# Optimization experiments

Measured on AMD Instinct MI355X. Metric: run time of the kernel, lower is better.

Reference implementation:

```python
import jax, jax.numpy as jnp
import numpy as np

B, H, W = 32, 768, 768
POS_THR = 0.1
NEG_RATIO = 3
TOPK_NO_POS = 500


def setup_inputs() -> dict:
    key = jax.random.key(0)
    k1, k2, k3 = jax.random.split(key, 3)
    pred = jax.random.uniform(k1, (B, H, W, 2), dtype=jnp.float32)
    region_scores = jax.random.uniform(k2, (B, H, W), dtype=jnp.float32) ** 16
    affinity_scores = jax.random.uniform(k3, (B, H, W), dtype=jnp.float32) ** 16
    return {"pred": pred, "region_scores": region_scores, "affinity_scores": affinity_scores}


def _single_image_loss(pre_loss, label):
    # Vectorized OHEM: replaces the per-sample Python loop + torch.topk.
    b = pre_loss.shape[0]
    loss = pre_loss.reshape(b, -1)   # [B, N]
    lab = label.reshape(b, -1)       # [B, N]
    n = loss.shape[1]
    pos = lab >= POS_THR             # [B, N] bool
    p = jnp.sum(pos, axis=1)         # positive pixel count per sample
    pos_sum = jnp.sum(jnp.where(pos, loss, 0.0), axis=1)
    posi_loss = jnp.where(p > 0, pos_sum / jnp.maximum(p, 1).astype(loss.dtype), 0.0)
    # Negatives sorted descending; -inf pushes positives to the tail.
    # When p == 0 the mask is all-False so this sorts the full loss vector,
    # matching torch.topk(pre_loss[i], 500).
    neg_vals = jnp.where(pos, -jnp.inf, loss)
    sorted_desc = jnp.flip(jnp.sort(neg_vals, axis=1), axis=1)
    nn = n - p                       # negative count
    # mean of all negatives when nn < 3p == mean of top-min(nn,3p); else top-3p
    k = jnp.where(p > 0, jnp.minimum(nn, NEG_RATIO * p), TOPK_NO_POS)
    csum = jnp.cumsum(jnp.where(jnp.isfinite(sorted_desc), sorted_desc, 0.0), axis=1)
    topk_sum = jnp.take_along_axis(csum, jnp.maximum(k - 1, 0)[:, None], axis=1)[:, 0]
    nega_loss = jnp.where(k > 0, topk_sum / jnp.maximum(k, 1).astype(loss.dtype), 0.0)
    return jnp.sum(posi_loss + nega_loss)


def reference(pred, region_scores, affinity_scores):
    p_gh = pred[..., 0]
    p_gah = pred[..., 1]
    loss1 = (p_gh - region_scores) ** 2   # MSELoss(reduction='none')
    loss2 = (p_gah - affinity_scores) ** 2
    char_loss = _single_image_loss(loss1, region_scores)
    affi_loss = _single_image_loss(loss2, affinity_scores)
    b = pred.shape[0]
    return char_loss / b + affi_loss / b
```

## Files before the change

### kernel.cpp

```cpp
#include <hip/hip_runtime.h>


constexpr int   BATCH   = 32;
constexpr int   NPS     = 768 * 768;
constexpr int   CH2     = BATCH * 2;
constexpr int   EPB     = 8192;
constexpr int   BX      = NPS / EPB;
constexpr float POS_THR_F = 0.1f;
constexpr unsigned TOPK_NO_POS = 500u;
constexpr int   NB1     = 2048;
constexpr int   CAP     = 131072;
constexpr int   CAPB    = 1024;

__global__ __launch_bounds__(256, 8) void k_hist(
    const float4* __restrict__ pred4,
    const float4* __restrict__ reg4,
    const float4* __restrict__ aff4,
    unsigned* __restrict__ h1c,
    unsigned* __restrict__ pcnt, float* __restrict__ psum)
{
    __shared__ unsigned sc0[NB1], sc1[NB1];
    __shared__ unsigned wpc[8];
    __shared__ float    wps[8];
    for (int j = threadIdx.x; j < NB1; j += 256) { sc0[j] = 0u; sc1[j] = 0u; }
    __syncthreads();

    const int  b   = blockIdx.y;
    const int  tid = threadIdx.x;
    constexpr int ITERS = EPB / 1024;
    long idx4 = (((long)b * NPS + (long)blockIdx.x * EPB) >> 2) + tid;

    unsigned pc0 = 0, pc1 = 0;
    float    ps0 = 0.f, ps1 = 0.f;

    for (int i = 0; i < ITERS; ++i) {
        const float4 r  = reg4[idx4];
        const float4 a  = aff4[idx4];
        const float4 pA = pred4[idx4 * 2];
        const float4 pB = pred4[idx4 * 2 + 1];
#define DO_PIX(RR, AA, PG, PA) do {                                           \
        float d0 = (PG) - (RR); float v0 = d0 * d0;                           \
        if ((RR) >= POS_THR_F) { pc0++; ps0 += v0; }                          \
        else atomicAdd(&sc0[__float_as_uint(v0) >> 19], 1u);                  \
        float d1 = (PA) - (AA); float v1 = d1 * d1;                           \
        if ((AA) >= POS_THR_F) { pc1++; ps1 += v1; }                          \
        else atomicAdd(&sc1[__float_as_uint(v1) >> 19], 1u);                  \
    } while (0)
        DO_PIX(r.x, a.x, pA.x, pA.y);
        DO_PIX(r.y, a.y, pA.z, pA.w);
        DO_PIX(r.z, a.z, pB.x, pB.y);
        DO_PIX(r.w, a.w, pB.z, pB.w);
#undef DO_PIX
        idx4 += 256;
    }
    __syncthreads();

    for (int j = tid; j < NB1; j += 256) {
        unsigned c0 = sc0[j];
        if (c0) atomicAdd(&h1c[(b*2+0)*NB1 + j], c0);
        unsigned c1 = sc1[j];
        if (c1) atomicAdd(&h1c[(b*2+1)*NB1 + j], c1);
    }
    for (int o = 32; o > 0; o >>= 1) {
        pc0 += __shfl_down(pc0, o); ps0 += __shfl_down(ps0, o);
        pc1 += __shfl_down(pc1, o); ps1 += __shfl_down(ps1, o);
    }
    const int wid = tid >> 6, lane = tid & 63;
    if (lane == 0) { wpc[wid] = pc0; wps[wid] = ps0; wpc[4+wid] = pc1; wps[4+wid] = ps1; }
    __syncthreads();
    if (tid == 0) {
        unsigned t0 = 0, t1 = 0; float s0 = 0.f, s1 = 0.f;
        for (int q = 0; q < 4; ++q) { t0 += wpc[q]; s0 += wps[q]; t1 += wpc[4+q]; s1 += wps[4+q]; }
        atomicAdd(&pcnt[b*2+0], t0); unsafeAtomicAdd(&psum[b*2+0], s0);
        atomicAdd(&pcnt[b*2+1], t1); unsafeAtomicAdd(&psum[b*2+1], s1);
    }
}

template<int NBINS>
__device__ __forceinline__ void select_counts(
    const unsigned* cnt, unsigned k, unsigned& outBin, unsigned& outRem)
{
    constexpr int PER = NBINS / 256;
    const int t = threadIdx.x;
    unsigned lc[PER];
#pragma unroll
    for (int j = 0; j < PER; ++j) lc[j] = cnt[t*PER + j];
    unsigned lsum = 0;
#pragma unroll
    for (int j = 0; j < PER; ++j) lsum += lc[j];

    __shared__ unsigned part[256];
    __shared__ unsigned s_bin, s_rem;
    part[t] = lsum;
    __syncthreads();
    for (int off = 1; off < 256; off <<= 1) {
        unsigned v = (t + off < 256) ? part[t + off] : 0u;
        __syncthreads();
        part[t] += v;
        __syncthreads();
    }
    unsigned cum = (t + 1 < 256) ? part[t + 1] : 0u;
#pragma unroll
    for (int j = PER - 1; j >= 0; --j) {
        unsigned c = lc[j];
        if (cum < k && k <= cum + c) { s_bin = (unsigned)(t * PER + j); s_rem = k - cum; }
        cum += c;
    }
    __syncthreads();
    outBin = s_bin; outRem = s_rem;
}

__global__ __launch_bounds__(256) void k_scan1(
    const unsigned* __restrict__ h1c,
    const unsigned* __restrict__ pcnt, const float* __restrict__ psum,
    unsigned* __restrict__ T1, unsigned* __restrict__ rem1,
    unsigned* __restrict__ kk, float* __restrict__ posi)
{
    const int idx = blockIdx.x;
    const unsigned p  = pcnt[idx];
    const unsigned nn = (unsigned)NPS - p;
    const unsigned k  = p ? ((nn < 3u*p) ? nn : 3u*p) : TOPK_NO_POS;
    if (threadIdx.x == 0) {
        kk[idx]   = k;
        posi[idx] = p ? (psum[idx] / (float)p) : 0.0f;
    }
    if (k == 0u) {
        if (threadIdx.x == 0) { T1[idx] = 0xFFFFFFFFu; rem1[idx] = 0u; }
        return;
    }
    unsigned bin, rem;
    select_counts<NB1>(h1c + idx*NB1, k, bin, rem);
    if (threadIdx.x == 0) { T1[idx] = bin; rem1[idx] = rem; }
}

__global__ __launch_bounds__(256, 8) void k_compact(
    const float4* __restrict__ pred4,
    const float4* __restrict__ reg4,
    const float4* __restrict__ aff4,
    const unsigned* __restrict__ T1,
    float* __restrict__ cbuf, unsigned* __restrict__ ccnt,
    double* __restrict__ sumAbove)
{
    __shared__ float    lb0[CAPB], lb1[CAPB];
    __shared__ unsigned lcnt[2];
    __shared__ unsigned sbase[2];
    __shared__ float    wred[8];
    if (threadIdx.x < 2) lcnt[threadIdx.x] = 0u;
    __syncthreads();

    const int b = blockIdx.y;
    const unsigned t1r = T1[b*2+0], t1a = T1[b*2+1];
    const int tid = threadIdx.x, lane = tid & 63;
    float*    gb0 = cbuf + (size_t)(b*2+0) * CAP;
    float*    gb1 = cbuf + (size_t)(b*2+1) * CAP;
    unsigned* gc0 = ccnt + b*2+0;
    unsigned* gc1 = ccnt + b*2+1;
    float rs0 = 0.f, rs1 = 0.f;

    auto proc = [&](float tgt, float pg, unsigned t1, float& rs,
                    unsigned* lcnt_p, float* lbuf, unsigned* gcnt, float* gbuf) {
        if (tgt >= POS_THR_F) return;
        const float d = pg - tgt;
        const float v = d * d;
        const unsigned key = __float_as_uint(v) >> 19;
        if (key > t1) { rs += v; return; }
        if (key != t1) return;
        const unsigned long long m = __ballot(true);
        const int ldr = __ffsll(m) - 1;
        const unsigned pre = (unsigned)__popcll(m & ((1ull << lane) - 1ull));
        unsigned base = 0;
        if (lane == ldr) base = atomicAdd(lcnt_p, (unsigned)__popcll(m));
        base = __shfl(base, ldr);
        const unsigned ix = base + pre;
        if (ix < (unsigned)CAPB) lbuf[ix] = v;
        else { unsigned g = atomicAdd(gcnt, 1u); if (g < (unsigned)CAP) gbuf[g] = v; }
    };

    constexpr int ITERS = EPB / 1024;
    long idx4 = (((long)b * NPS + (long)blockIdx.x * EPB) >> 2) + tid;

    for (int i = 0; i < ITERS; ++i) {
        const float4 r  = reg4[idx4];
        const float4 a  = aff4[idx4];
        const float4 pA = pred4[idx4 * 2];
        const float4 pB = pred4[idx4 * 2 + 1];
        proc(r.x, pA.x, t1r, rs0, &lcnt[0], lb0, gc0, gb0);
        proc(r.y, pA.z, t1r, rs0, &lcnt[0], lb0, gc0, gb0);
        proc(r.z, pB.x, t1r, rs0, &lcnt[0], lb0, gc0, gb0);
        proc(r.w, pB.z, t1r, rs0, &lcnt[0], lb0, gc0, gb0);
        proc(a.x, pA.y, t1a, rs1, &lcnt[1], lb1, gc1, gb1);
        proc(a.y, pA.w, t1a, rs1, &lcnt[1], lb1, gc1, gb1);
        proc(a.z, pB.y, t1a, rs1, &lcnt[1], lb1, gc1, gb1);
        proc(a.w, pB.w, t1a, rs1, &lcnt[1], lb1, gc1, gb1);
        idx4 += 256;
    }
    __syncthreads();

    const unsigned lc0 = lcnt[0] < (unsigned)CAPB ? lcnt[0] : (unsigned)CAPB;
    const unsigned lc1 = lcnt[1] < (unsigned)CAPB ? lcnt[1] : (unsigned)CAPB;
    if (tid == 0)      sbase[0] = lc0 ? atomicAdd(gc0, lc0) : 0u;
    else if (tid == 1) sbase[1] = lc1 ? atomicAdd(gc1, lc1) : 0u;
    __syncthreads();
    for (unsigned i = tid; i < lc0; i += 256) {
        unsigned g = sbase[0] + i;
        if (g < (unsigned)CAP) gb0[g] = lb0[i];
    }
    for (unsigned i = tid; i < lc1; i += 256) {
        unsigned g = sbase[1] + i;
        if (g < (unsigned)CAP) gb1[g] = lb1[i];
    }
    for (int o = 32; o > 0; o >>= 1) { rs0 += __shfl_down(rs0, o); rs1 += __shfl_down(rs1, o); }
    const int wid = tid >> 6;
    if (lane == 0) { wred[wid] = rs0; wred[4+wid] = rs1; }
    __syncthreads();
    if (tid == 0) {
        float s0 = wred[0]+wred[1]+wred[2]+wred[3];
        float s1 = wred[4]+wred[5]+wred[6]+wred[7];
        unsafeAtomicAdd(&sumAbove[b*2+0], (double)s0);
        unsafeAtomicAdd(&sumAbove[b*2+1], (double)s1);
    }
}

__global__ __launch_bounds__(256) void k_refine(
    const float* __restrict__ cbuf, const unsigned* __restrict__ ccnt,
    const unsigned* __restrict__ T1, const unsigned* __restrict__ rem1,
    const unsigned* __restrict__ kk, const float* __restrict__ posi,
    const double* __restrict__ sumAbove,
    float* __restrict__ contrib)
{
    const int ch = blockIdx.x;
    const unsigned k = kk[ch];
    if (k == 0u) {
        if (threadIdx.x == 0) contrib[ch] = posi[ch];
        return;
    }
    unsigned cnt = ccnt[ch];
    if (cnt > (unsigned)CAP) cnt = (unsigned)CAP;
    const float* buf = cbuf + (size_t)ch * CAP;
    const int tid = threadIdx.x;

    __shared__ unsigned hA[NB1];
    __shared__ unsigned hB[256];
    __shared__ double   wsum[4];
    for (int j = tid; j < NB1; j += 256) hA[j] = 0u;
    __syncthreads();
    for (unsigned i = tid; i < cnt; i += 256) {
        const unsigned bt = __float_as_uint(buf[i]);
        atomicAdd(&hA[(bt >> 8) & 2047u], 1u);
    }
    __syncthreads();
    unsigned T2, rem2;
    select_counts<NB1>(hA, rem1[ch], T2, rem2);

    hB[tid] = 0u;
    __syncthreads();
    for (unsigned i = tid; i < cnt; i += 256) {
        const unsigned bt = __float_as_uint(buf[i]);
        if (((bt >> 8) & 2047u) == T2) atomicAdd(&hB[bt & 255u], 1u);
    }
    __syncthreads();
    unsigned T3, rem3;
    select_counts<256>(hB, rem2, T3, rem3);

    const float t = __uint_as_float((T1[ch] << 19) | (T2 << 8) | T3);
    double s = 0.0;
    for (unsigned i = tid; i < cnt; i += 256) {
        const float v = buf[i];
        if (v > t) s += (double)v;
    }
    for (int o = 32; o > 0; o >>= 1) s += __shfl_down(s, o);
    const int wid = tid >> 6, lane = tid & 63;
    if (lane == 0) wsum[wid] = s;
    __syncthreads();
    if (tid == 0) {
        const double stop = wsum[0] + wsum[1] + wsum[2] + wsum[3];
        const double nega = (sumAbove[ch] + stop + (double)rem3 * (double)t) / (double)k;
        contrib[ch] = (float)((double)posi[ch] + nega);
    }
}

__global__ void k_reduce(const float* __restrict__ contrib, float* __restrict__ out)
{
    double v = (double)contrib[threadIdx.x];
    for (int o = 32; o > 0; o >>= 1) v += __shfl_down(v, o);
    if (threadIdx.x == 0) out[0] = (float)(v / (double)BATCH);
}

extern "C" void kernel_launch(void* const* d_in, const int* in_sizes, int n_in,
                              void* d_out, int out_size, void* d_ws, size_t ws_size,
                              hipStream_t stream)
{
    (void)in_sizes; (void)n_in; (void)out_size; (void)ws_size;
    const float4* pred4 = (const float4*)d_in[0];
    const float4* reg4  = (const float4*)d_in[1];
    const float4* aff4  = (const float4*)d_in[2];

    char* w = (char*)d_ws;
    unsigned* h1c  = (unsigned*)w;
    unsigned* pcnt = h1c + (size_t)CH2 * NB1;
    float*    psum = (float*)(pcnt + CH2);
    unsigned* T1   = (unsigned*)(psum + CH2);
    unsigned* rem1 = T1 + CH2;
    unsigned* kk   = rem1 + CH2;
    float*    posi = (float*)(kk + CH2);
    float*    contrib = posi + CH2;
    unsigned* ccnt = (unsigned*)(contrib + CH2);
    double*   sumAbove = (double*)(ccnt + CH2);
    const size_t hdr_bytes = (size_t)((char*)(sumAbove + CH2) - w);

    float* cbuf = (float*)(w + ((size_t)1 << 20));

    hipMemsetAsync(d_ws, 0, hdr_bytes, stream);

    dim3 grid(BX, BATCH);
    k_hist<<<grid, 256, 0, stream>>>(pred4, reg4, aff4, h1c, pcnt, psum);
    k_scan1<<<CH2, 256, 0, stream>>>(h1c, pcnt, psum, T1, rem1, kk, posi);
    k_compact<<<grid, 256, 0, stream>>>(pred4, reg4, aff4, T1, cbuf, ccnt, sumAbove);
    k_refine<<<CH2, 256, 0, stream>>>(cbuf, ccnt, T1, rem1, kk, posi, sumAbove, contrib);
    k_reduce<<<1, 64, 0, stream>>>(contrib, (float*)d_out);
}
```

Baseline: 415.0 us.

## Double-buffer streaming loads, enlarge per-block work, fuse final reduction into refine

The histogram and compaction kernels now prefetch the next iteration's float4 inputs while processing the current ones, and each block handles twice as many elements with a lower occupancy hint. The goal is to hide global-load latency and halve the number of per-block shared-histogram flushes and atomics. The separate single-block reduction kernel is removed: the last finishing refine block, detected with an atomic counter, sums the per-channel contributions and writes the output. This saves one launch but adds register pressure and halves the grid size, which may reduce latency hiding.

```diff
diff --git a/kernel.cpp b/kernel.cpp
--- a/kernel.cpp
+++ b/kernel.cpp
@@ -4,7 +4,7 @@
 constexpr int   BATCH   = 32;
 constexpr int   NPS     = 768 * 768;
 constexpr int   CH2     = BATCH * 2;
-constexpr int   EPB     = 8192;
+constexpr int   EPB     = 16384;
 constexpr int   BX      = NPS / EPB;
 constexpr float POS_THR_F = 0.1f;
 constexpr unsigned TOPK_NO_POS = 500u;
@@ -12,7 +12,7 @@
 constexpr int   CAP     = 131072;
 constexpr int   CAPB    = 1024;
 
-__global__ __launch_bounds__(256, 8) void k_hist(
+__global__ __launch_bounds__(256, 6) void k_hist(
     const float4* __restrict__ pred4,
     const float4* __restrict__ reg4,
     const float4* __restrict__ aff4,
@@ -33,11 +33,15 @@
     unsigned pc0 = 0, pc1 = 0;
     float    ps0 = 0.f, ps1 = 0.f;
 
+    float4 r = reg4[idx4], a = aff4[idx4];
+    float4 pA = pred4[idx4 * 2], pB = pred4[idx4 * 2 + 1];
+
     for (int i = 0; i < ITERS; ++i) {
-        const float4 r  = reg4[idx4];
-        const float4 a  = aff4[idx4];
-        const float4 pA = pred4[idx4 * 2];
-        const float4 pB = pred4[idx4 * 2 + 1];
+        float4 rn, an, pAn, pBn;
+        if (i + 1 < ITERS) {
+            const long nx = idx4 + 256;
+            rn = reg4[nx]; an = aff4[nx]; pAn = pred4[nx * 2]; pBn = pred4[nx * 2 + 1];
+        }
 #define DO_PIX(RR, AA, PG, PA) do {                                           \
         float d0 = (PG) - (RR); float v0 = d0 * d0;                           \
         if ((RR) >= POS_THR_F) { pc0++; ps0 += v0; }                          \
@@ -51,7 +55,7 @@
         DO_PIX(r.z, a.z, pB.x, pB.y);
         DO_PIX(r.w, a.w, pB.z, pB.w);
 #undef DO_PIX
-        idx4 += 256;
+        idx4 += 256; r = rn; a = an; pA = pAn; pB = pBn;
     }
     __syncthreads();
 
@@ -133,7 +137,7 @@
     if (threadIdx.x == 0) { T1[idx] = bin; rem1[idx] = rem; }
 }
 
-__global__ __launch_bounds__(256, 8) void k_compact(
+__global__ __launch_bounds__(256, 6) void k_compact(
     const float4* __restrict__ pred4,
     const float4* __restrict__ reg4,
     const float4* __restrict__ aff4,
@@ -179,11 +183,15 @@
     constexpr int ITERS = EPB / 1024;
     long idx4 = (((long)b * NPS + (long)blockIdx.x * EPB) >> 2) + tid;
 
+    float4 r = reg4[idx4], a = aff4[idx4];
+    float4 pA = pred4[idx4 * 2], pB = pred4[idx4 * 2 + 1];
+
     for (int i = 0; i < ITERS; ++i) {
-        const float4 r  = reg4[idx4];
-        const float4 a  = aff4[idx4];
-        const float4 pA = pred4[idx4 * 2];
-        const float4 pB = pred4[idx4 * 2 + 1];
+        float4 rn, an, pAn, pBn;
+        if (i + 1 < ITERS) {
+            const long nx = idx4 + 256;
+            rn = reg4[nx]; an = aff4[nx]; pAn = pred4[nx * 2]; pBn = pred4[nx * 2 + 1];
+        }
         proc(r.x, pA.x, t1r, rs0, &lcnt[0], lb0, gc0, gb0);
         proc(r.y, pA.z, t1r, rs0, &lcnt[0], lb0, gc0, gb0);
         proc(r.z, pB.x, t1r, rs0, &lcnt[0], lb0, gc0, gb0);
@@ -192,7 +200,7 @@
         proc(a.y, pA.w, t1a, rs1, &lcnt[1], lb1, gc1, gb1);
         proc(a.z, pB.y, t1a, rs1, &lcnt[1], lb1, gc1, gb1);
         proc(a.w, pB.w, t1a, rs1, &lcnt[1], lb1, gc1, gb1);
-        idx4 += 256;
+        idx4 += 256; r = rn; a = an; pA = pAn; pB = pBn;
     }
     __syncthreads();
 
@@ -226,18 +234,32 @@
     const unsigned* __restrict__ T1, const unsigned* __restrict__ rem1,
     const unsigned* __restrict__ kk, const float* __restrict__ posi,
     const double* __restrict__ sumAbove,
-    float* __restrict__ contrib)
+    float* __restrict__ contrib,
+    unsigned* __restrict__ done, float* __restrict__ out)
 {
     const int ch = blockIdx.x;
+    const int tid = threadIdx.x;
     const unsigned k = kk[ch];
+
+    auto finish = [&](float cval) {
+        contrib[ch] = cval;
+        __threadfence();
+        const unsigned d = atomicAdd(done, 1u);
+        if (d == (unsigned)CH2 - 1u) {
+            __threadfence();
+            double acc = 0.0;
+            for (int i = 0; i < CH2; ++i) acc += (double)contrib[i];
+            out[0] = (float)(acc / (double)BATCH);
+        }
+    };
+
     if (k == 0u) {
-        if (threadIdx.x == 0) contrib[ch] = posi[ch];
+        if (tid == 0) finish(posi[ch]);
         return;
     }
     unsigned cnt = ccnt[ch];
     if (cnt > (unsigned)CAP) cnt = (unsigned)CAP;
     const float* buf = cbuf + (size_t)ch * CAP;
-    const int tid = threadIdx.x;
 
     __shared__ unsigned hA[NB1];
     __shared__ unsigned hB[256];
@@ -275,15 +297,8 @@
     if (tid == 0) {
         const double stop = wsum[0] + wsum[1] + wsum[2] + wsum[3];
         const double nega = (sumAbove[ch] + stop + (double)rem3 * (double)t) / (double)k;
-        contrib[ch] = (float)((double)posi[ch] + nega);
-    }
-}
-
-__global__ void k_reduce(const float* __restrict__ contrib, float* __restrict__ out)
-{
-    double v = (double)contrib[threadIdx.x];
-    for (int o = 32; o > 0; o >>= 1) v += __shfl_down(v, o);
-    if (threadIdx.x == 0) out[0] = (float)(v / (double)BATCH);
+        finish((float)((double)posi[ch] + nega));
+    }
 }
 
 extern "C" void kernel_launch(void* const* d_in, const int* in_sizes, int n_in,
@@ -306,7 +321,8 @@
     float*    contrib = posi + CH2;
     unsigned* ccnt = (unsigned*)(contrib + CH2);
     double*   sumAbove = (double*)(ccnt + CH2);
-    const size_t hdr_bytes = (size_t)((char*)(sumAbove + CH2) - w);
+    unsigned* done = (unsigned*)(sumAbove + CH2);
+    const size_t hdr_bytes = (size_t)((char*)(done + 1) - w);
 
     float* cbuf = (float*)(w + ((size_t)1 << 20));
 
@@ -316,6 +332,6 @@
     k_hist<<<grid, 256, 0, stream>>>(pred4, reg4, aff4, h1c, pcnt, psum);
     k_scan1<<<CH2, 256, 0, stream>>>(h1c, pcnt, psum, T1, rem1, kk, posi);
     k_compact<<<grid, 256, 0, stream>>>(pred4, reg4, aff4, T1, cbuf, ccnt, sumAbove);
-    k_refine<<<CH2, 256, 0, stream>>>(cbuf, ccnt, T1, rem1, kk, posi, sumAbove, contrib);
-    k_reduce<<<1, 64, 0, stream>>>(contrib, (float*)d_out);
-}
+    k_refine<<<CH2, 256, 0, stream>>>(cbuf, ccnt, T1, rem1, kk, posi, sumAbove,
+                                      contrib, done, (float*)d_out);
+}
```

Measured after the change: 401.6 us. 3.2% less time.
